# Kernel optimization log

Hardware: AMD Instinct MI355X
Metric: run time of the kernel (lower is better)

Reference implementation:

```python
import jax, jax.numpy as jnp
import numpy as np
import math

EMBED_DIMS = 256
NUM_LANDMARKS = 40  # hard-coded k=40 in the original module
B, N = 2, 8192


def setup_inputs() -> dict:
    key = jax.random.key(0)
    ks = jax.random.split(key, 9)
    C = EMBED_DIMS
    w = lambda k: jax.random.normal(k, (C, C), dtype=jnp.float32) * 0.02
    b = lambda k: jax.random.normal(k, (C,), dtype=jnp.float32) * 0.02
    return {
        "query": jax.random.normal(ks[0], (B, N, C), dtype=jnp.float32),
        "Wq": w(ks[1]), "bq": b(ks[2]),
        "Wk": w(ks[3]), "bk": b(ks[4]),
        "Wv": w(ks[5]), "bv": b(ks[6]),
        "Wo": w(ks[7]), "bo": b(ks[8]),
    }


def reference(query, Wq, bq, Wk, bk, Wv, bv, Wo, bo):
    # key = value = identity = query (defaults in the original forward)
    C = query.shape[-1]
    scaling = math.sqrt(C)

    q = query @ Wq.T + bq  # [B, N, C]
    k = query @ Wk.T + bk
    v = query @ Wv.T + bv

    # Full similarity only to score keys: score_m[b, m] = sum_n sim_nm[b, n, m]
    sim_nm = jnp.einsum('bnc,bmc->bnm', q, k) / scaling  # [B, N, N]
    score_m = sim_nm.sum(axis=1)                          # [B, N]

    _, top_idx = jax.lax.top_k(score_m, NUM_LANDMARKS)    # [B, 40]
    selected = jnp.take_along_axis(k, top_idx[:, :, None], axis=1)  # [B, 40, C]

    sim_qn = jax.nn.softmax(jnp.einsum('bnc,bkc->bnk', q, selected) / scaling, axis=-1)  # [B, N, 40]
    sim_km = jax.nn.softmax(jnp.einsum('bmc,bkc->bmk', k, selected) / scaling, axis=-1)  # [B, N, 40]

    sim_qk = jnp.einsum('bnk,bmk->bnm', sim_qn, sim_km)   # [B, N, N]
    out = jnp.einsum('bnm,bmc->bnc', sim_qk, v)           # [B, N, C]
    out = out @ Wo.T + bo
    return query + out  # identity residual; dropouts are identity at p=0
```

## Files before the change

### kernel.cpp

```cpp
#include <hip/hip_runtime.h>
#include <cstddef>
#include <cstdint>

#define BATCH 2
#define SEQ 8192
#define CH 256
#define NLM 40
#define NLMP 48
#define MROWS (BATCH * SEQ)
#define INV_SCALE 0.0625f
#define NCBLK 256

typedef unsigned short ushort_t;
typedef __attribute__((ext_vector_type(8))) short short8;
typedef __attribute__((ext_vector_type(4))) float floatx4;

__device__ __forceinline__ ushort_t f2bf(float f) {
    unsigned int u = __float_as_uint(f);
    u += 0x7FFFu + ((u >> 16) & 1u);
    return (ushort_t)(u >> 16);
}
__device__ __forceinline__ float bf2f(ushort_t u) {
    return __uint_as_float(((unsigned)u) << 16);
}

__device__ __forceinline__ void gload_lds16(const ushort_t* g, ushort_t* l) {
    __builtin_amdgcn_global_load_lds(
        (const __attribute__((address_space(1))) unsigned int*)g,
        (__attribute__((address_space(3))) unsigned int*)l, 16, 0, 0);
}

__global__ __launch_bounds__(256) void convert_colsum(const float* __restrict__ x,
                                                      ushort_t* __restrict__ xbf,
                                                      float* __restrict__ partial) {
    __shared__ float red[4][256];
    const int b = blockIdx.y;
    const int r0 = blockIdx.x * 32;
    const int t = threadIdx.x;
    const int c4 = (t & 63) * 4;
    const int rg = t >> 6;
    const float* base = x + ((size_t)b * SEQ + r0) * 256;
    ushort_t* obase = xbf + ((size_t)b * SEQ + r0) * 256;
    float4 s = {0.f, 0.f, 0.f, 0.f};
#pragma unroll
    for (int i = 0; i < 8; i++) {
        const int r = rg + i * 4;
        const float4 a = *(const float4*)&base[(size_t)r * 256 + c4];
        uint2 o;
        o.x = f2bf(a.x) | ((unsigned)f2bf(a.y) << 16);
        o.y = f2bf(a.z) | ((unsigned)f2bf(a.w) << 16);
        *(uint2*)&obase[(size_t)r * 256 + c4] = o;
        s.x += a.x; s.y += a.y; s.z += a.z; s.w += a.w;
    }
    *(float4*)&red[rg][c4] = s;
    __syncthreads();
    const float tot = red[0][t] + red[1][t] + red[2][t] + red[3][t];
    partial[((size_t)b * NCBLK + blockIdx.x) * 256 + t] = tot;
}

__global__ __launch_bounds__(1024) void ws_kernel(const float* __restrict__ partial,
                                                  const float* __restrict__ Wq,
                                                  const float* __restrict__ bq,
                                                  const float* __restrict__ Wk,
                                                  float* __restrict__ ws,
                                                  float* __restrict__ tmat) {
    const int b = blockIdx.x;
    __shared__ float xs[256];
    __shared__ float qs[256];
    __shared__ float ppart[4][256];
    const int t = threadIdx.x;
    {
        float* tz = tmat + (size_t)b * NLM * 256;
        for (int i = t; i < NLM * 256; i += 1024) tz[i] = 0.f;
    }
    {
        const int c = t & 255, qd = t >> 8;
        const float* pb = partial + ((size_t)b * NCBLK + qd * 64) * 256 + c;
        float a = 0.f;
#pragma unroll 8
        for (int i = 0; i < 64; i++) a += pb[(size_t)i * 256];
        ppart[qd][c] = a;
    }
    __syncthreads();
    if (t < 256) xs[t] = ppart[0][t] + ppart[1][t] + ppart[2][t] + ppart[3][t];
    __syncthreads();
    const int lane = t & 63, w = t >> 6;
    {
        float4 wq[16];
#pragma unroll
        for (int g = 0; g < 16; g++)
            wq[g] = *(const float4*)&Wq[(size_t)(w * 16 + g) * 256 + lane * 4];
        const float4 x4 = *(const float4*)&xs[lane * 4];
#pragma unroll
        for (int g = 0; g < 16; g++) {
            const int o = w * 16 + g;
            float d = wq[g].x * x4.x + wq[g].y * x4.y + wq[g].z * x4.z + wq[g].w * x4.w;
#pragma unroll
            for (int off = 32; off >= 1; off >>= 1) d += __shfl_down(d, off);
            if (lane == 0) qs[o] = d + 8192.0f * bq[o];
        }
    }
    __syncthreads();
    const int c = t & 255, part = t >> 8;
    float a = 0.f;
#pragma unroll 16
    for (int o = part * 64; o < part * 64 + 64; o++)
        a += Wk[(size_t)o * 256 + c] * qs[o];
    ppart[part][c] = a;
    __syncthreads();
    if (t < 256)
        ws[b * 256 + t] = ppart[0][t] + ppart[1][t] + ppart[2][t] + ppart[3][t];
}

__global__ __launch_bounds__(256) void gemm_qkv_score(const ushort_t* __restrict__ xbf,
                                                      const float* __restrict__ Wq,
                                                      const float* __restrict__ Wk,
                                                      const float* __restrict__ Wv,
                                                      const float* __restrict__ bq,
                                                      const float* __restrict__ bk,
                                                      const float* __restrict__ bv,
                                                      ushort_t* __restrict__ qkv,
                                                      const float* __restrict__ query,
                                                      const float* __restrict__ ws,
                                                      float* __restrict__ score) {
    __shared__ __align__(16) char smem[24576];
    ushort_t* As = (ushort_t*)smem;
    ushort_t* Bs = (ushort_t*)(smem + 16384);
    ushort_t* Es = (ushort_t*)smem;
    const int lin = blockIdx.x;
    const int wg = (lin & 7) * 256 + (lin >> 3);
    const int bx = wg & 3;
    const int by = (wg >> 2) & 127;
    const int z = wg >> 9;
    const int t = threadIdx.x;
    const int lane = t & 63;
    const int w = t >> 6;

    if (z == 3) {
        const int blk = by * 4 + bx;
#pragma unroll
        for (int i = 0; i < 8; i++) {
            const int g = blk * 32 + i * 4 + w;
            const int b = g >> 13;
            const int m = g & 8191;
            const float4 kv = *(const float4*)&query[(size_t)g * 256 + lane * 4];
            const float4 qs = *(const float4*)&ws[b * 256 + lane * 4];
            float d = kv.x * qs.x + kv.y * qs.y + kv.z * qs.z + kv.w * qs.w;
#pragma unroll
            for (int off = 32; off >= 1; off >>= 1) d += __shfl_down(d, off);
            if (lane == 0) score[(size_t)b * SEQ + m] = d * INV_SCALE;
        }
        return;
    }

    const float* __restrict__ W = (z == 0) ? Wq : (z == 1) ? Wk : Wv;
    const float* __restrict__ bias = (z == 0) ? bq : (z == 1) ? bk : bv;
    ushort_t* __restrict__ out = qkv + (size_t)z * MROWS * 256;
    const int o0 = bx * 64;
    const int m0 = by * 128;
    const int quad = lane >> 4;
    const int l16 = lane & 15;
    const int xsw = l16 & 7;

    floatx4 acc[2][4];
#pragma unroll
    for (int rt = 0; rt < 2; rt++)
#pragma unroll
        for (int ct = 0; ct < 4; ct++) acc[rt][ct] = (floatx4){0.f, 0.f, 0.f, 0.f};

    for (int kc = 0; kc < 256; kc += 64) {
#pragma unroll
        for (int q = 0; q < 4; q++) {
            const int r0 = w * 32 + q * 8;
            gload_lds16(&xbf[(size_t)(m0 + r0 + (lane >> 3)) * 256 + kc +
                             (((lane & 7) ^ (lane >> 3)) * 8)],
                        &As[r0 * 64]);
        }
#pragma unroll
        for (int u = 0; u < 2; u++) {
            const int cid = t + u * 256;
            const int row = cid >> 3;
            const int cch = cid & 7;
            const float* wp = &W[(size_t)(o0 + row) * 256 + kc + cch * 8];
            const float4 a = *(const float4*)wp;
            const float4 c = *(const float4*)(wp + 4);
            uint4 o;
            o.x = f2bf(a.x) | ((unsigned)f2bf(a.y) << 16);
            o.y = f2bf(a.z) | ((unsigned)f2bf(a.w) << 16);
            o.z = f2bf(c.x) | ((unsigned)f2bf(c.y) << 16);
            o.w = f2bf(c.z) | ((unsigned)f2bf(c.w) << 16);
            *(uint4*)&Bs[row * 64 + ((cch ^ (row & 7)) * 8)] = o;
        }
        __syncthreads();
#pragma unroll
        for (int s = 0; s < 2; s++) {
            short8 a[2], bf[4];
#pragma unroll
            for (int rt = 0; rt < 2; rt++)
                a[rt] = *(const short8*)&As[(w * 32 + rt * 16 + l16) * 64 +
                                            (((s * 4 + quad) ^ xsw) * 8)];
#pragma unroll
            for (int ct = 0; ct < 4; ct++)
                bf[ct] = *(const short8*)&Bs[(ct * 16 + l16) * 64 +
                                             (((s * 4 + quad) ^ xsw) * 8)];
#pragma unroll
            for (int rt = 0; rt < 2; rt++)
#pragma unroll
                for (int ct = 0; ct < 4; ct++)
                    acc[rt][ct] = __builtin_amdgcn_mfma_f32_16x16x32_bf16(
                        a[rt], bf[ct], acc[rt][ct], 0, 0, 0);
        }
        __syncthreads();
    }

#pragma unroll
    for (int rt = 0; rt < 2; rt++) {
#pragma unroll
        for (int ct = 0; ct < 4; ct++) {
            const int col = ct * 16 + l16;
            const float bb = bias[o0 + col];
#pragma unroll
            for (int reg = 0; reg < 4; reg++) {
                const int row = w * 32 + rt * 16 + quad * 4 + reg;
                Es[row * 72 + col] = f2bf(acc[rt][ct][reg] + bb);
            }
        }
    }
    __syncthreads();
#pragma unroll
    for (int u = 0; u < 4; u++) {
        const int cid = t + u * 256;
        const int row = cid >> 3;
        const int off = (cid & 7) * 8;
        *(uint4*)&out[(size_t)(m0 + row) * 256 + o0 + off] =
            *(const uint4*)&Es[row * 72 + off];
    }
}

__global__ __launch_bounds__(1024) void topk_gather(const float* __restrict__ score,
                                                    const ushort_t* __restrict__ kmat,
                                                    ushort_t* __restrict__ sel) {
    const int b = blockIdx.x;
    const int t = threadIdx.x;
    __shared__ unsigned hist[256];
    __shared__ unsigned sPrefix, sMask, sRem, sNeq;
    __shared__ int sNgt;
    __shared__ int top[NLM];
    __shared__ unsigned topkey[NLM];

    unsigned key[8];
#pragma unroll
    for (int j = 0; j < 8; j++) {
        const unsigned u = __float_as_uint(score[(size_t)b * SEQ + t + j * 1024]);
        key[j] = u ^ (unsigned)(((int)u >> 31) | 0x80000000);
    }
    if (t == 0) { sPrefix = 0; sMask = 0; sRem = NLM; sNgt = 0; sNeq = 0; }

    for (int lvl = 0; lvl < 4; lvl++) {
        const int shift = 24 - 8 * lvl;
        if (t < 256) hist[t] = 0;
        __syncthreads();
        const unsigned pfx = sPrefix, msk = sMask;
#pragma unroll
        for (int j = 0; j < 8; j++)
            if (((key[j] ^ pfx) & msk) == 0)
                atomicAdd(&hist[(key[j] >> shift) & 255u], 1u);
        __syncthreads();
        if (t < 64) {
            unsigned sfx = hist[t * 4] + hist[t * 4 + 1] + hist[t * 4 + 2] + hist[t * 4 + 3];
#pragma unroll
            for (int off = 1; off < 64; off <<= 1) {
                const unsigned o = __shfl_down(sfx, off);
                if (t + off < 64) sfx += o;
            }
            const unsigned rem = sRem;
            const unsigned long long mk = __ballot(sfx >= rem);
            const int gstar = 63 - __builtin_clzll(mk);
            unsigned S1 = __shfl(sfx, (gstar + 1) & 63);
            if (gstar == 63) S1 = 0u;
            if (t == 0) {
                int d = gstar * 4 + 3;
                unsigned cum = S1;
                for (; d > gstar * 4; d--) { if (cum + hist[d] >= rem) break; cum += hist[d]; }
                sRem = rem - cum;
                sPrefix |= ((unsigned)d) << shift;
                sMask |= 255u << shift;
            }
        }
        __syncthreads();
    }
    const unsigned K40 = sPrefix;
    const unsigned rem = sRem;
    const int ngt = NLM - (int)rem;

#pragma unroll
    for (int j = 0; j < 8; j++) {
        if (key[j] > K40) {
            const int slot = atomicAdd(&sNgt, 1);
            top[slot] = t + j * 1024; topkey[slot] = key[j];
        } else if (key[j] == K40) {
            const unsigned e = atomicAdd(&sNeq, 1u);
            if (e < rem) {
                const int slot = ngt + (int)e;
                top[slot] = t + j * 1024; topkey[slot] = key[j];
            }
        }
    }
    __syncthreads();

    if (t < 64) {
        unsigned long long c = (t < NLM)
            ? ((((unsigned long long)(~topkey[t])) << 32) | (unsigned)top[t])
            : 0xFFFFFFFFFFFFFFFFull;
#pragma unroll
        for (int kk = 2; kk <= 64; kk <<= 1) {
#pragma unroll
            for (int j = kk >> 1; j >= 1; j >>= 1) {
                const unsigned long long o = __shfl_xor(c, j);
                const bool takeMin = ((t & kk) == 0) == ((t & j) == 0);
                const bool less = c < o;
                c = (takeMin == less) ? c : o;
            }
        }
        if (t < NLM) top[t] = (int)(c & 0xFFFFFFFFu);
    }
    __syncthreads();

    for (int f = t; f < NLMP * 256; f += 1024) {
        const int j = f >> 8;
        const int cc = f & 255;
        sel[(size_t)b * NLMP * 256 + f] =
            (j < NLM) ? kmat[((size_t)b * SEQ + top[j]) * 256 + cc] : (ushort_t)0;
    }
}

__global__ __launch_bounds__(256, 4) void sim_fused(const ushort_t* __restrict__ qbf,
                                                    const ushort_t* __restrict__ kbf,
                                                    const ushort_t* __restrict__ vbf,
                                                    const ushort_t* __restrict__ sel,
                                                    float* __restrict__ simq,
                                                    float* __restrict__ tmat) {
    __shared__ __align__(16) char smem[43008];
    float (*Ps)[40]  = (float(*)[40])smem;
    ushort_t* Vs     = (ushort_t*)(smem + 10240);
    const int b = blockIdx.y;
    const int n0 = blockIdx.x * 64;
    const int t = threadIdx.x;
    const int lane = t & 63;
    const int w = t >> 6;
    const int quad = lane >> 4;
    const int l16 = lane & 15;
    const ushort_t* __restrict__ A = (blockIdx.z == 0) ? qbf : kbf;
    const ushort_t* __restrict__ Arow = A + ((size_t)b * SEQ + n0 + w * 16 + l16) * 256;
    const ushort_t* __restrict__ Sb = sel + (size_t)b * NLMP * 256 + (size_t)l16 * 256;

    floatx4 acc[3];
#pragma unroll
    for (int ct = 0; ct < 3; ct++) acc[ct] = (floatx4){0.f, 0.f, 0.f, 0.f};

#pragma unroll
    for (int ks = 0; ks < 8; ks++) {
        const int ko = ks * 32 + quad * 8;
        const short8 a  = *(const short8*)&Arow[ko];
        const short8 b0 = *(const short8*)&Sb[ko];
        const short8 b1 = *(const short8*)&Sb[16 * 256 + ko];
        const short8 b2 = *(const short8*)&Sb[32 * 256 + ko];
        acc[0] = __builtin_amdgcn_mfma_f32_16x16x32_bf16(a, b0, acc[0], 0, 0, 0);
        acc[1] = __builtin_amdgcn_mfma_f32_16x16x32_bf16(a, b1, acc[1], 0, 0, 0);
        acc[2] = __builtin_amdgcn_mfma_f32_16x16x32_bf16(a, b2, acc[2], 0, 0, 0);
    }

    const bool v2ok = (l16 < 8);
    float p0[4], p1[4], p2[4];
#pragma unroll
    for (int reg = 0; reg < 4; reg++) {
        const float l0 = acc[0][reg] * INV_SCALE;
        const float l1 = acc[1][reg] * INV_SCALE;
        const float l2 = acc[2][reg] * INV_SCALE;
        float m = fmaxf(l0, l1);
        if (v2ok) m = fmaxf(m, l2);
        m = fmaxf(m, __shfl_xor(m, 1));
        m = fmaxf(m, __shfl_xor(m, 2));
        m = fmaxf(m, __shfl_xor(m, 4));
        m = fmaxf(m, __shfl_xor(m, 8));
        const float e0 = expf(l0 - m);
        const float e1 = expf(l1 - m);
        const float e2 = v2ok ? expf(l2 - m) : 0.f;
        float s = e0 + e1 + e2;
        s += __shfl_xor(s, 1);
        s += __shfl_xor(s, 2);
        s += __shfl_xor(s, 4);
        s += __shfl_xor(s, 8);
        const float inv = 1.f / s;
        p0[reg] = e0 * inv; p1[reg] = e1 * inv; p2[reg] = e2 * inv;
    }

    const int row0 = w * 16 + quad * 4;
    if (blockIdx.z == 0) {
        float* __restrict__ dst = &simq[((size_t)b * SEQ + n0 + row0) * NLM];
#pragma unroll
        for (int reg = 0; reg < 4; reg++) {
            float* __restrict__ d2 = dst + reg * NLM;
            d2[l16] = p0[reg];
            d2[16 + l16] = p1[reg];
            if (v2ok) d2[32 + l16] = p2[reg];
        }
        return;
    }

#pragma unroll
    for (int reg = 0; reg < 4; reg++) {
        Ps[row0 + reg][l16] = p0[reg];
        Ps[row0 + reg][16 + l16] = p1[reg];
        if (v2ok) Ps[row0 + reg][32 + l16] = p2[reg];
    }
#pragma unroll
    for (int u = 0; u < 8; u++) {
        gload_lds16(&vbf[((size_t)b * SEQ + n0 + w * 2 + u * 8 + (lane >> 5)) * 256 +
                         (lane & 31) * 8],
                    &Vs[(w * 2 + u * 8) * 256]);
    }
    __syncthreads();

    float tac[40];
#pragma unroll
    for (int j = 0; j < 40; j++) tac[j] = 0.f;

#pragma unroll 2
    for (int m = 0; m < 64; m++) {
        const float vv = bf2f(Vs[m * 256 + t]);
#pragma unroll
        for (int j4 = 0; j4 < 10; j4++) {
            const float4 p = *(const float4*)&Ps[m][j4 * 4];
            tac[j4 * 4 + 0] = fmaf(p.x, vv, tac[j4 * 4 + 0]);
            tac[j4 * 4 + 1] = fmaf(p.y, vv, tac[j4 * 4 + 1]);
            tac[j4 * 4 + 2] = fmaf(p.z, vv, tac[j4 * 4 + 2]);
            tac[j4 * 4 + 3] = fmaf(p.w, vv, tac[j4 * 4 + 3]);
        }
    }
#pragma unroll
    for (int j = 0; j < 40; j++)
        atomicAdd(&tmat[(size_t)b * NLM * 256 + j * 256 + t], tac[j]);
}

__global__ __launch_bounds__(512) void out_fused(const float* __restrict__ simq,
                                                 const float* __restrict__ tmat,
                                                 const float* __restrict__ Wo,
                                                 const float* __restrict__ bias,
                                                 const float* __restrict__ resid,
                                                 float* __restrict__ out) {
    __shared__ __align__(16) char smem[75776];
    float* Ps = (float*)smem;
    ushort_t* Ac = (ushort_t*)(smem + 10240);
    ushort_t* Bs = (ushort_t*)(smem + 43008);

    const int t = threadIdx.x;
    const int m0 = blockIdx.x * 64;
    const int b = blockIdx.x >> 7;
    const int lane = t & 63;
    const int w = t >> 6;
    const int quad = lane >> 4;
    const int l16 = lane & 15;
    const int xsw = l16 & 7;
    const int rt_base = (w & 3) * 16;
    const int cg_base = (w >> 2) * 8;

    for (int f = t; f < 64 * NLM; f += 512)
        Ps[f] = simq[(size_t)m0 * NLM + f];
    __syncthreads();

    {
        const int col = t & 255;
        const int r0 = (t >> 8) * 32;
        const float* __restrict__ Tb = tmat + (size_t)b * NLM * 256;
        float tc[40];
#pragma unroll
        for (int l = 0; l < 40; l++) tc[l] = Tb[l * 256 + col];
        const int chunk = col >> 3;
#pragma unroll
        for (int r = 0; r < 32; r++) {
            const int rr = r0 + r;
            float a = 0.f;
#pragma unroll
            for (int j4 = 0; j4 < 10; j4++) {
                const float4 p = *(const float4*)&Ps[rr * 40 + j4 * 4];
                a = fmaf(p.x, tc[j4 * 4 + 0], a);
                a = fmaf(p.y, tc[j4 * 4 + 1], a);
                a = fmaf(p.z, tc[j4 * 4 + 2], a);
                a = fmaf(p.w, tc[j4 * 4 + 3], a);
            }
            const int pch = (chunk & ~7) | ((chunk & 7) ^ (rr & 7));
            Ac[rr * 256 + pch * 8 + (col & 7)] = f2bf(a);
        }
    }

    floatx4 acc[8];
#pragma unroll
    for (int ct = 0; ct < 8; ct++) acc[ct] = (floatx4){0.f, 0.f, 0.f, 0.f};

    for (int kc = 0; kc < 256; kc += 64) {
#pragma unroll
        for (int u = 0; u < 4; u++) {
            const int cid = t + u * 512;
            const int row = cid >> 3;
            const int cch = cid & 7;
            const float* wp = &Wo[(size_t)row * 256 + kc + cch * 8];
            const float4 a = *(const float4*)wp;
            const float4 c = *(const float4*)(wp + 4);
            uint4 o;
            o.x = f2bf(a.x) | ((unsigned)f2bf(a.y) << 16);
            o.y = f2bf(a.z) | ((unsigned)f2bf(a.w) << 16);
            o.z = f2bf(c.x) | ((unsigned)f2bf(c.y) << 16);
            o.w = f2bf(c.z) | ((unsigned)f2bf(c.w) << 16);
            *(uint4*)&Bs[row * 64 + ((cch ^ (row & 7)) * 8)] = o;
        }
        __syncthreads();
#pragma unroll
        for (int s = 0; s < 2; s++) {
            const short8 a = *(const short8*)&Ac[(rt_base + l16) * 256 +
                                                 ((kc >> 3) + ((s * 4 + quad) ^ xsw)) * 8];
#pragma unroll
            for (int ct = 0; ct < 8; ct++) {
                const short8 bf = *(const short8*)&Bs[((cg_base + ct) * 16 + l16) * 64 +
                                                      (((s * 4 + quad) ^ xsw) * 8)];
                acc[ct] = __builtin_amdgcn_mfma_f32_16x16x32_bf16(a, bf, acc[ct], 0, 0, 0);
            }
        }
        __syncthreads();
    }

#pragma unroll
    for (int ct = 0; ct < 8; ct++) {
        const int col = (cg_base + ct) * 16 + l16;
        const float bb = bias[col];
#pragma unroll
        for (int reg = 0; reg < 4; reg++) {
            const int row = rt_base + quad * 4 + reg;
            const size_t idx = (size_t)(m0 + row) * 256 + col;
            out[idx] = (acc[ct][reg] + bb) + resid[idx];
        }
    }
}

extern "C" void kernel_launch(void* const* d_in, const int* in_sizes, int n_in,
                              void* d_out, int out_size, void* d_ws, size_t ws_size,
                              hipStream_t stream) {
    const float* query = (const float*)d_in[0];
    const float* Wq = (const float*)d_in[1];
    const float* bq = (const float*)d_in[2];
    const float* Wk = (const float*)d_in[3];
    const float* bk = (const float*)d_in[4];
    const float* Wv = (const float*)d_in[5];
    const float* bv = (const float*)d_in[6];
    const float* Wo = (const float*)d_in[7];
    const float* bo = (const float*)d_in[8];
    float* out = (float*)d_out;

    char* p = (char*)d_ws;
    float* simq  = (float*)p;            p += (size_t)MROWS * NLM * 4;
    ushort_t* selbf = (ushort_t*)p;      p += (size_t)BATCH * NLMP * 256 * 2;
    float* tmat  = (float*)p;            p += (size_t)BATCH * NLM * 256 * 4;
    float* partial = (float*)p;          p += (size_t)BATCH * NCBLK * 256 * 4;
    float* ws    = (float*)p;            p += (size_t)BATCH * 256 * 4;
    float* score = (float*)p;            p += (size_t)BATCH * SEQ * 4;
    ushort_t* qkv = (ushort_t*)p;        p += (size_t)3 * MROWS * 256 * 2;
    ushort_t* xbf = (ushort_t*)p;        p += (size_t)MROWS * 256 * 2;
    ushort_t* qbf = qkv;
    ushort_t* kbf = qkv + (size_t)MROWS * 256;
    ushort_t* vbf = qkv + (size_t)2 * MROWS * 256;

    const dim3 blk(256);

    convert_colsum<<<dim3(SEQ / 32, BATCH), blk, 0, stream>>>(query, xbf, partial);
    ws_kernel<<<dim3(BATCH), dim3(1024), 0, stream>>>(partial, Wq, bq, Wk, ws, tmat);

    gemm_qkv_score<<<dim3(2048), blk, 0, stream>>>(
        xbf, Wq, Wk, Wv, bq, bk, bv, qkv, query, ws, score);

    topk_gather<<<dim3(BATCH), dim3(1024), 0, stream>>>(score, kbf, selbf);

    sim_fused<<<dim3(SEQ / 64, BATCH, 2), blk, 0, stream>>>(qbf, kbf, vbf, selbf, simq, tmat);

    out_fused<<<dim3(MROWS / 64), dim3(512), 0, stream>>>(simq, tmat, Wo, bo, query, out);
}
```

Baseline: 175.3 us.

## Pre-convert Wo to bf16 once and halve out_fused row tile

Wo is converted to bf16 once inside ws_kernel and stored in workspace. out_fused then streams it straight into LDS with direct global-to-LDS loads instead of reconverting fp32 weights in every block. out_fused also moves from 64-row to 32-row tiles, which doubles the grid and cuts LDS use to improve occupancy. The cost is that Wo is loaded twice as often in total and each wave issues fewer MFMAs, so there is less reuse per load.

```diff
diff --git a/kernel.cpp b/kernel.cpp
--- a/kernel.cpp
+++ b/kernel.cpp
@@ -62,8 +62,10 @@
                                                   const float* __restrict__ Wq,
                                                   const float* __restrict__ bq,
                                                   const float* __restrict__ Wk,
+                                                  const float* __restrict__ Wo,
                                                   float* __restrict__ ws,
-                                                  float* __restrict__ tmat) {
+                                                  float* __restrict__ tmat,
+                                                  ushort_t* __restrict__ wobf) {
     const int b = blockIdx.x;
     __shared__ float xs[256];
     __shared__ float qs[256];
@@ -72,6 +74,20 @@
     {
         float* tz = tmat + (size_t)b * NLM * 256;
         for (int i = t; i < NLM * 256; i += 1024) tz[i] = 0.f;
+    }
+    {
+        const int base = (b * 1024 + t) * 32;
+#pragma unroll
+        for (int i = 0; i < 32; i += 8) {
+            const float4 a = *(const float4*)&Wo[base + i];
+            const float4 c = *(const float4*)&Wo[base + i + 4];
+            uint4 o;
+            o.x = f2bf(a.x) | ((unsigned)f2bf(a.y) << 16);
+            o.y = f2bf(a.z) | ((unsigned)f2bf(a.w) << 16);
+            o.z = f2bf(c.x) | ((unsigned)f2bf(c.y) << 16);
+            o.w = f2bf(c.z) | ((unsigned)f2bf(c.w) << 16);
+            *(uint4*)&wobf[base + i] = o;
+        }
     }
     {
         const int c = t & 255, qd = t >> 8;
@@ -445,40 +461,40 @@
 
 __global__ __launch_bounds__(512) void out_fused(const float* __restrict__ simq,
                                                  const float* __restrict__ tmat,
-                                                 const float* __restrict__ Wo,
+                                                 const ushort_t* __restrict__ wobf,
                                                  const float* __restrict__ bias,
                                                  const float* __restrict__ resid,
                                                  float* __restrict__ out) {
-    __shared__ __align__(16) char smem[75776];
+    __shared__ __align__(16) char smem[54272];
     float* Ps = (float*)smem;
-    ushort_t* Ac = (ushort_t*)(smem + 10240);
-    ushort_t* Bs = (ushort_t*)(smem + 43008);
+    ushort_t* Ac = (ushort_t*)(smem + 5120);
+    ushort_t* Bs = (ushort_t*)(smem + 21504);
 
     const int t = threadIdx.x;
-    const int m0 = blockIdx.x * 64;
-    const int b = blockIdx.x >> 7;
+    const int m0 = blockIdx.x * 32;
+    const int b = blockIdx.x >> 8;
     const int lane = t & 63;
     const int w = t >> 6;
     const int quad = lane >> 4;
     const int l16 = lane & 15;
     const int xsw = l16 & 7;
-    const int rt_base = (w & 3) * 16;
-    const int cg_base = (w >> 2) * 8;
-
-    for (int f = t; f < 64 * NLM; f += 512)
+    const int rt_base = (w & 1) * 16;
+    const int cg_base = (w >> 1) * 4;
+
+    for (int f = t; f < 32 * NLM; f += 512)
         Ps[f] = simq[(size_t)m0 * NLM + f];
     __syncthreads();
 
     {
         const int col = t & 255;
-        const int r0 = (t >> 8) * 32;
+        const int r0 = (t >> 8) * 16;
         const float* __restrict__ Tb = tmat + (size_t)b * NLM * 256;
         float tc[40];
 #pragma unroll
         for (int l = 0; l < 40; l++) tc[l] = Tb[l * 256 + col];
         const int chunk = col >> 3;
 #pragma unroll
-        for (int r = 0; r < 32; r++) {
+        for (int r = 0; r < 16; r++) {
             const int rr = r0 + r;
             float a = 0.f;
 #pragma unroll
@@ -494,25 +510,17 @@
         }
     }
 
-    floatx4 acc[8];
-#pragma unroll
-    for (int ct = 0; ct < 8; ct++) acc[ct] = (floatx4){0.f, 0.f, 0.f, 0.f};
+    floatx4 acc[4];
+#pragma unroll
+    for (int ct = 0; ct < 4; ct++) acc[ct] = (floatx4){0.f, 0.f, 0.f, 0.f};
 
     for (int kc = 0; kc < 256; kc += 64) {
 #pragma unroll
-        for (int u = 0; u < 4; u++) {
-            const int cid = t + u * 512;
-            const int row = cid >> 3;
-            const int cch = cid & 7;
-            const float* wp = &Wo[(size_t)row * 256 + kc + cch * 8];
-            const float4 a = *(const float4*)wp;
-            const float4 c = *(const float4*)(wp + 4);
-            uint4 o;
-            o.x = f2bf(a.x) | ((unsigned)f2bf(a.y) << 16);
-            o.y = f2bf(a.z) | ((unsigned)f2bf(a.w) << 16);
-            o.z = f2bf(c.x) | ((unsigned)f2bf(c.y) << 16);
-            o.w = f2bf(c.z) | ((unsigned)f2bf(c.w) << 16);
-            *(uint4*)&Bs[row * 64 + ((cch ^ (row & 7)) * 8)] = o;
+        for (int q = 0; q < 4; q++) {
+            const int r0 = w * 32 + q * 8;
+            gload_lds16(&wobf[(size_t)(r0 + (lane >> 3)) * 256 + kc +
+                              (((lane & 7) ^ (lane >> 3)) * 8)],
+                        &Bs[r0 * 64]);
         }
         __syncthreads();
 #pragma unroll
@@ -520,7 +528,7 @@
             const short8 a = *(const short8*)&Ac[(rt_base + l16) * 256 +
                                                  ((kc >> 3) + ((s * 4 + quad) ^ xsw)) * 8];
 #pragma unroll
-            for (int ct = 0; ct < 8; ct++) {
+            for (int ct = 0; ct < 4; ct++) {
                 const short8 bf = *(const short8*)&Bs[((cg_base + ct) * 16 + l16) * 64 +
                                                       (((s * 4 + quad) ^ xsw) * 8)];
                 acc[ct] = __builtin_amdgcn_mfma_f32_16x16x32_bf16(a, bf, acc[ct], 0, 0, 0);
@@ -530,7 +538,7 @@
     }
 
 #pragma unroll
-    for (int ct = 0; ct < 8; ct++) {
+    for (int ct = 0; ct < 4; ct++) {
         const int col = (cg_base + ct) * 16 + l16;
         const float bb = bias[col];
 #pragma unroll
@@ -563,6 +571,7 @@
     float* partial = (float*)p;          p += (size_t)BATCH * NCBLK * 256 * 4;
     float* ws    = (float*)p;            p += (size_t)BATCH * 256 * 4;
     float* score = (float*)p;            p += (size_t)BATCH * SEQ * 4;
+    ushort_t* wobf = (ushort_t*)p;       p += (size_t)256 * 256 * 2;
     ushort_t* qkv = (ushort_t*)p;        p += (size_t)3 * MROWS * 256 * 2;
     ushort_t* xbf = (ushort_t*)p;        p += (size_t)MROWS * 256 * 2;
     ushort_t* qbf = qkv;
@@ -572,7 +581,7 @@
     const dim3 blk(256);
 
     convert_colsum<<<dim3(SEQ / 32, BATCH), blk, 0, stream>>>(query, xbf, partial);
-    ws_kernel<<<dim3(BATCH), dim3(1024), 0, stream>>>(partial, Wq, bq, Wk, ws, tmat);
+    ws_kernel<<<dim3(BATCH), dim3(1024), 0, stream>>>(partial, Wq, bq, Wk, Wo, ws, tmat, wobf);
 
     gemm_qkv_score<<<dim3(2048), blk, 0, stream>>>(
         xbf, Wq, Wk, Wv, bq, bk, bv, qkv, query, ws, score);
@@ -581,5 +590,5 @@
 
     sim_fused<<<dim3(SEQ / 64, BATCH, 2), blk, 0, stream>>>(qbf, kbf, vbf, selbf, simq, tmat);
 
-    out_fused<<<dim3(MROWS / 64), dim3(512), 0, stream>>>(simq, tmat, Wo, bo, query, out);
-}
+    out_fused<<<dim3(MROWS / 32), dim3(512), 0, stream>>>(simq, tmat, wobf, bo, query, out);
+}
```

Measured after the change: 177.4 us (median of 2 runs). Within noise of the previous version (+1.2%).
